# Kernel tuning notes

Hardware: AMD Instinct MI355X
Metric: run time of the kernel (lower is better)

The kernel has to match this reference:

```python
import jax, jax.numpy as jnp
import numpy as np
from jax import lax

N, G, L, D, E, STEPS = 65536, 128, 512, 128, 262144, 6
C = 2 * D  # concat dim (input_dim + output_dim)


def setup_inputs() -> dict:
    key = jax.random.key(0)
    ks = jax.random.split(key, 12)
    sD = 1.0 / float(np.sqrt(D))
    sC = 1.0 / float(np.sqrt(C))
    return {
        "x": jax.random.normal(ks[0], (N, D), jnp.float32),
        "edge_index": jax.random.randint(ks[1], (2, E), 0, N, dtype=jnp.int32),
        "edge_weight": jax.random.uniform(ks[2], (E,), jnp.float32),
        "batch": (jnp.arange(N) // L).astype(jnp.int32),  # sorted graph ids, L nodes/graph
        "ggnn_w": jax.random.normal(ks[3], (STEPS, D, D), jnp.float32) * sD,
        "gru_wih": jax.random.normal(ks[4], (3 * D, D), jnp.float32) * sD,
        "gru_whh": jax.random.normal(ks[5], (3 * D, D), jnp.float32) * sD,
        "gru_bih": jnp.zeros((3 * D,), jnp.float32),
        "gru_bhh": jnp.zeros((3 * D,), jnp.float32),
        "conv1_w": jax.random.normal(ks[6], (D, D, 3), jnp.float32) * sD,
        "conv1_b": jnp.zeros((D,), jnp.float32),
        "conv2_w": jax.random.normal(ks[7], (D, D, 1), jnp.float32) * sD,
        "conv2_b": jnp.zeros((D,), jnp.float32),
        "convc1_w": jax.random.normal(ks[8], (C, C, 3), jnp.float32) * sC,
        "convc1_b": jnp.zeros((C,), jnp.float32),
        "convc2_w": jax.random.normal(ks[9], (C, C, 1), jnp.float32) * sC,
        "convc2_b": jnp.zeros((C,), jnp.float32),
        "bn1_g": jnp.ones((D,), jnp.float32),
        "bn1_b": jnp.zeros((D,), jnp.float32),
        "bn2_g": jnp.ones((C,), jnp.float32),
        "bn2_b": jnp.zeros((C,), jnp.float32),
        "mlpy_w": jax.random.normal(ks[10], (2, D), jnp.float32) * sD,
        "mlpy_b": jnp.zeros((2,), jnp.float32),
        "mlpz_w": jax.random.normal(ks[11], (2, C), jnp.float32) * sC,
        "mlpz_b": jnp.zeros((2,), jnp.float32),
    }


def _gru(m, h, wih, whh, bih, bhh):
    gx = m @ wih.T + bih
    gh = h @ whh.T + bhh
    xr, xz, xn = jnp.split(gx, 3, axis=-1)
    hr, hz, hn = jnp.split(gh, 3, axis=-1)
    r = jax.nn.sigmoid(xr + hr)
    z = jax.nn.sigmoid(xz + hz)
    n = jnp.tanh(xn + r * hn)
    return (1.0 - z) * n + z * h


def _conv1d(x, w, b):  # x [G,Cin,L], w [Cout,Cin,K]
    y = lax.conv_general_dilated(x, w, (1,), "VALID", dimension_numbers=("NCH", "OIH", "NCH"))
    return y + b[None, :, None]


def _maxpool(x, k, s):
    return lax.reduce_window(x, -jnp.inf, lax.max, (1, 1, k), (1, 1, s), "VALID")


def _bn(x, g, b):  # training-mode BatchNorm1d over (N, L) per channel
    mean = x.mean(axis=(0, 2), keepdims=True)
    var = x.var(axis=(0, 2), keepdims=True)
    return (x - mean) * lax.rsqrt(var + 1e-5) * g[None, :, None] + b[None, :, None]


def reference(x, edge_index, edge_weight, batch, ggnn_w, gru_wih, gru_whh, gru_bih,
              gru_bhh, conv1_w, conv1_b, conv2_w, conv2_b, convc1_w, convc1_b,
              convc2_w, convc2_b, bn1_g, bn1_b, bn2_g, bn2_b, mlpy_w, mlpy_b,
              mlpz_w, mlpz_b):
    src, dst = edge_index[0], edge_index[1]

    # GatedGraphConv: per layer linear -> weighted message scatter-add -> GRU update
    def step(h, w):
        m = h @ w
        agg = jax.ops.segment_sum(m[src] * edge_weight[:, None], dst, num_segments=N)
        return _gru(agg, h, gru_wih, gru_whh, gru_bih, gru_bhh), None

    h, _ = lax.scan(step, x, ggnn_w)

    # de_batchify_graphs: one fused scatter into zero-padded [G, L, *] tensor
    counts = jax.ops.segment_sum(jnp.ones((N,), jnp.int32), batch, num_segments=G)
    offsets = jnp.cumsum(counts) - counts
    pos = jnp.arange(N) - offsets[batch]
    x_i = jnp.zeros((G, L, D), x.dtype).at[batch, pos].set(x)
    h_i = jnp.zeros((G, L, D), h.dtype).at[batch, pos].set(h)
    c_i = jnp.concatenate([h_i, x_i], axis=-1)  # [G, L, 2D]

    hT = h_i.transpose(0, 2, 1)  # [G, D, L]
    Y1 = _maxpool(jax.nn.relu(_bn(_conv1d(hT, conv1_w, conv1_b), bn1_g, bn1_b)), 3, 2)
    Y2 = _maxpool(jax.nn.relu(_bn(_conv1d(Y1, conv2_w, conv2_b), bn1_g, bn1_b)), 2, 2).transpose(0, 2, 1)
    cT = c_i.transpose(0, 2, 1)  # [G, 2D, L]
    Z1 = _maxpool(jax.nn.relu(_bn(_conv1d(cT, convc1_w, convc1_b), bn2_g, bn2_b)), 3, 2)
    Z2 = _maxpool(jax.nn.relu(_bn(_conv1d(Z1, convc2_w, convc2_b), bn2_g, bn2_b)), 2, 2).transpose(0, 2, 1)

    before_avg = (Y2 @ mlpy_w.T + mlpy_b) * (Z2 @ mlpz_w.T + mlpz_b)  # [G, L', 2]
    return before_avg.mean(axis=1)  # [G, 2]
```

## Files before the change

### kernel.cpp

```cpp
#include <hip/hip_runtime.h>
#include <math.h>

#define NN 65536
#define GG 128
#define LL 512
#define DD 128
#define EE 262144
#define NSTEPS 6
#define CC 256
#define L1 510
#define P1 254
#define P2 127

typedef __attribute__((ext_vector_type(8))) short s8bf;
typedef __attribute__((ext_vector_type(4))) float f4acc;

__device__ __forceinline__ unsigned short f2bf(float x) {
  unsigned u = __float_as_uint(x);
  unsigned r = u + 0x7FFFu + ((u >> 16) & 1u);
  return (unsigned short)(r >> 16);
}
__device__ __forceinline__ float bf2f(unsigned short h) {
  return __uint_as_float(((unsigned)h) << 16);
}
__device__ __forceinline__ unsigned short f2bf_sel(float x, int lo_sel) {
  unsigned short hi = f2bf(x);
  if (!lo_sel) return hi;
  return f2bf(x - bf2f(hi));
}
__device__ __forceinline__ uint2 pack4bf(float4 v, int lo_sel) {
  unsigned short s0 = f2bf_sel(v.x, lo_sel), s1 = f2bf_sel(v.y, lo_sel);
  unsigned short s2 = f2bf_sel(v.z, lo_sel), s3 = f2bf_sel(v.w, lo_sel);
  uint2 pk; pk.x = (unsigned)s0 | ((unsigned)s1 << 16);
  pk.y = (unsigned)s2 | ((unsigned)s3 << 16);
  return pk;
}

__global__ __launch_bounds__(256) void k_prep(
    const float* __restrict__ wih, const float* __restrict__ whh,
    const float* __restrict__ gw,
    const float* __restrict__ w1, const float* __restrict__ wc1,
    const float* __restrict__ w2, const float* __restrict__ wc2,
    unsigned short* __restrict__ wihCh, unsigned short* __restrict__ wihCl,
    unsigned short* __restrict__ whhCh, unsigned short* __restrict__ whhCl,
    unsigned short* __restrict__ gwTh, unsigned short* __restrict__ gwTl,
    unsigned short* __restrict__ c1h, unsigned short* __restrict__ c1l,
    unsigned short* __restrict__ cc1h, unsigned short* __restrict__ cc1l,
    unsigned short* __restrict__ c2h, unsigned short* __restrict__ c2l,
    unsigned short* __restrict__ cc2h, unsigned short* __restrict__ cc2l) {
  int i = blockIdx.x * 256 + threadIdx.x;
  if (i < 49152) {
    float v = wih[i];
    unsigned short h_ = f2bf(v);
    wihCh[i] = h_; wihCl[i] = f2bf(v - bf2f(h_));
    float u = whh[i];
    unsigned short h2 = f2bf(u);
    whhCh[i] = h2; whhCl[i] = f2bf(u - bf2f(h2));
  }
  if (i < 98304) {
    int s = i >> 14; int r = i & 16383; int c = r >> 7; int k = r & 127;
    float v = gw[(s << 14) + k * 128 + c];
    unsigned short h_ = f2bf(v);
    gwTh[i] = h_; gwTl[i] = f2bf(v - bf2f(h_));
  }
  if (i < 49152) {
    int ci = i & 127; int r = i >> 7; int co = r & 127; int tap = r >> 7;
    float v = w1[(co * 128 + ci) * 3 + tap];
    unsigned short h_ = f2bf(v);
    c1h[i] = h_; c1l[i] = f2bf(v - bf2f(h_));
  }
  if (i < 196608) {
    int ci = i & 255; int r = i >> 8; int co = r & 255; int tap = r >> 8;
    float v = wc1[(co * 256 + ci) * 3 + tap];
    unsigned short h_ = f2bf(v);
    cc1h[i] = h_; cc1l[i] = f2bf(v - bf2f(h_));
  }
  if (i < 16384) {
    float v = w2[i];
    unsigned short h_ = f2bf(v);
    c2h[i] = h_; c2l[i] = f2bf(v - bf2f(h_));
  }
  if (i < 65536) {
    float v = wc2[i];
    unsigned short h_ = f2bf(v);
    cc2h[i] = h_; cc2l[i] = f2bf(v - bf2f(h_));
  }
}

__global__ __launch_bounds__(256) void k_castx(const float* __restrict__ x,
                                               unsigned short* __restrict__ xH,
                                               unsigned short* __restrict__ xL) {
  int i = blockIdx.x * 256 + threadIdx.x;
  const float4* x4 = (const float4*)x;
  float4 a = x4[i * 2 + 0];
  float4 b = x4[i * 2 + 1];
  uint2 ha = pack4bf(a, 0), hb = pack4bf(b, 0);
  uint2 la = pack4bf(a, 1), lb = pack4bf(b, 1);
  uint4 hv; hv.x = ha.x; hv.y = ha.y; hv.z = hb.x; hv.w = hb.y;
  uint4 lv; lv.x = la.x; lv.y = la.y; lv.z = lb.x; lv.w = lb.y;
  *(uint4*)&xH[i * 8] = hv;
  *(uint4*)&xL[i * 8] = lv;
}

__global__ __launch_bounds__(256) void k_hist(const int* __restrict__ dst, int* __restrict__ cnt) {
  int e = blockIdx.x * 256 + threadIdx.x;
  if (e < EE) atomicAdd(&cnt[dst[e]], 1);
}

__global__ __launch_bounds__(1024) void k_scan(const int* __restrict__ cnt,
                                               int* __restrict__ rowptr,
                                               int* __restrict__ cursor) {
  __shared__ int part[1024];
  int t = threadIdx.x;
  int base = t * 64;
  int s = 0;
  for (int i = 0; i < 64; i++) s += cnt[base + i];
  part[t] = s;
  __syncthreads();
  for (int off = 1; off < 1024; off <<= 1) {
    int v = part[t];
    int u = (t >= off) ? part[t - off] : 0;
    __syncthreads();
    part[t] = v + u;
    __syncthreads();
  }
  int run = part[t] - s;
  for (int i = 0; i < 64; i++) {
    rowptr[base + i] = run;
    cursor[base + i] = run;
    run += cnt[base + i];
  }
  if (t == 1023) rowptr[NN] = run;
}

__global__ __launch_bounds__(256) void k_fill(const int* __restrict__ src,
                                              const int* __restrict__ dst,
                                              const float* __restrict__ ew,
                                              int* __restrict__ cursor,
                                              int* __restrict__ col,
                                              float* __restrict__ wgt) {
  int e = blockIdx.x * 256 + threadIdx.x;
  if (e < EE) {
    int d = dst[e];
    int p = atomicAdd(&cursor[d], 1);
    col[p] = src[e];
    wgt[p] = ew[e];
  }
}

__global__ __launch_bounds__(256, 4) void k_gemm_mfma(
    const unsigned short* __restrict__ Ah, const unsigned short* __restrict__ Al,
    const unsigned short* __restrict__ Wh, const unsigned short* __restrict__ Wl,
    float* __restrict__ Cout) {
  __shared__ __attribute__((aligned(16))) unsigned short As[64 * 136];
  int t = threadIdx.x;
  int r0 = blockIdx.x * 64;
  int wv = t >> 6, lane = t & 63;
  int ln = lane & 15, q = lane >> 4;
  f4acc acc[4][2];
#pragma unroll
  for (int mt = 0; mt < 4; mt++)
#pragma unroll
    for (int nt = 0; nt < 2; nt++) acc[mt][nt] = (f4acc)0.f;

  for (int p = 0; p < 3; p++) {
    if (p != 1) {
      const unsigned short* S = (p == 2) ? Al : Ah;
      if (p) __syncthreads();
#pragma unroll
      for (int it = 0; it < 4; it++) {
        int v8 = it * 256 + t;
        int row = v8 >> 4, k = (v8 & 15) * 8;
        *(uint4*)&As[row * 136 + k] = *(const uint4*)&S[(r0 + row) * 128 + k];
      }
      __syncthreads();
    }
    const unsigned short* W = (p == 1) ? Wl : Wh;
#pragma unroll
    for (int k0 = 0; k0 < 128; k0 += 32) {
      s8bf af[4], bf[2];
#pragma unroll
      for (int nt = 0; nt < 2; nt++)
        bf[nt] = *(const s8bf*)&W[(wv * 32 + nt * 16 + ln) * 128 + k0 + q * 8];
#pragma unroll
      for (int mt = 0; mt < 4; mt++)
        af[mt] = *(const s8bf*)&As[(mt * 16 + ln) * 136 + k0 + q * 8];
#pragma unroll
      for (int mt = 0; mt < 4; mt++)
#pragma unroll
        for (int nt = 0; nt < 2; nt++)
          acc[mt][nt] = __builtin_amdgcn_mfma_f32_16x16x32_bf16(af[mt], bf[nt], acc[mt][nt], 0, 0, 0);
    }
  }
#pragma unroll
  for (int mt = 0; mt < 4; mt++)
#pragma unroll
    for (int nt = 0; nt < 2; nt++)
#pragma unroll
      for (int reg = 0; reg < 4; reg++) {
        int r = r0 + mt * 16 + q * 4 + reg;
        Cout[r * 128 + wv * 32 + nt * 16 + ln] = acc[mt][nt][reg];
      }
}

__global__ __launch_bounds__(256) void k_gather(const float* __restrict__ m,
                                                const int* __restrict__ rowptr,
                                                const int* __restrict__ col,
                                                const float* __restrict__ wgt,
                                                unsigned short* __restrict__ aggH,
                                                unsigned short* __restrict__ aggL) {
  int t = threadIdx.x;
  int n = blockIdx.x * 8 + (t >> 5);
  int c4 = t & 31;
  const float4* m4 = (const float4*)m;
  int s0 = rowptr[n], s1 = rowptr[n + 1];
  float ax = 0.f, ay = 0.f, az = 0.f, aw = 0.f;
  int e = s0;
  for (; e + 2 <= s1; e += 2) {
    int cA = col[e], cB = col[e + 1];
    float wA = wgt[e], wB = wgt[e + 1];
    float4 vA = m4[cA * 32 + c4];
    float4 vB = m4[cB * 32 + c4];
    ax += vA.x * wA + vB.x * wB;
    ay += vA.y * wA + vB.y * wB;
    az += vA.z * wA + vB.z * wB;
    aw += vA.w * wA + vB.w * wB;
  }
  if (e < s1) {
    int cA = col[e];
    float wA = wgt[e];
    float4 vA = m4[cA * 32 + c4];
    ax += vA.x * wA; ay += vA.y * wA; az += vA.z * wA; aw += vA.w * wA;
  }
  unsigned short h0 = f2bf(ax), h1 = f2bf(ay), h2 = f2bf(az), h3 = f2bf(aw);
  unsigned short l0 = f2bf(ax - bf2f(h0)), l1 = f2bf(ay - bf2f(h1));
  unsigned short l2 = f2bf(az - bf2f(h2)), l3 = f2bf(aw - bf2f(h3));
  uint2 hpk, lpk;
  hpk.x = (unsigned)h0 | ((unsigned)h1 << 16); hpk.y = (unsigned)h2 | ((unsigned)h3 << 16);
  lpk.x = (unsigned)l0 | ((unsigned)l1 << 16); lpk.y = (unsigned)l2 | ((unsigned)l3 << 16);
  int base = n * 128 + c4 * 4;
  *(uint2*)&aggH[base] = hpk;
  *(uint2*)&aggL[base] = lpk;
}

__global__ __launch_bounds__(256, 2) void k_gru_mfma(
    const unsigned short* __restrict__ aggH, const unsigned short* __restrict__ aggL,
    const unsigned short* __restrict__ hinH, const unsigned short* __restrict__ hinL,
    const unsigned short* __restrict__ wihCh, const unsigned short* __restrict__ wihCl,
    const unsigned short* __restrict__ whhCh, const unsigned short* __restrict__ whhCl,
    const float* __restrict__ bih, const float* __restrict__ bhh,
    unsigned short* __restrict__ houtH, unsigned short* __restrict__ houtL) {
  __shared__ __attribute__((aligned(16))) unsigned short As[2 * 64 * 136];
  int t = threadIdx.x;
  int r0 = blockIdx.x * 64;
  int d0 = blockIdx.y * 64;
  int wv = t >> 6, lane = t & 63;
  int ln = lane & 15, q = lane >> 4;
  f4acc acc[4][6];
#pragma unroll
  for (int mt = 0; mt < 4; mt++)
#pragma unroll
    for (int tg = 0; tg < 6; tg++) acc[mt][tg] = (f4acc)0.f;

  for (int p = 0; p < 3; p++) {
    if (p != 1) {
      const unsigned short* s0 = (p == 2) ? aggL : aggH;
      const unsigned short* s1 = (p == 2) ? hinL : hinH;
      if (p) __syncthreads();
#pragma unroll
      for (int it = 0; it < 8; it++) {
        int v8 = it * 256 + t;
        int mat = v8 >> 10;
        int row = (v8 >> 4) & 63, k = (v8 & 15) * 8;
        const unsigned short* S = mat ? s1 : s0;
        *(uint4*)&As[mat * 8704 + row * 136 + k] = *(const uint4*)&S[(r0 + row) * 128 + k];
      }
      __syncthreads();
    }
    const unsigned short* wx = (p == 1) ? wihCl : wihCh;
    const unsigned short* wh = (p == 1) ? whhCl : whhCh;
#pragma unroll
    for (int k0 = 0; k0 < 128; k0 += 32) {
      s8bf af[2][4], bfr[6];
#pragma unroll
      for (int tg = 0; tg < 6; tg++) {
        int gate = (tg < 3) ? tg : tg - 3;
        const unsigned short* W = (tg < 3) ? wx : wh;
        bfr[tg] = *(const s8bf*)&W[(gate * 128 + d0 + wv * 16 + ln) * 128 + k0 + q * 8];
      }
#pragma unroll
      for (int mat = 0; mat < 2; mat++)
#pragma unroll
        for (int mt = 0; mt < 4; mt++)
          af[mat][mt] = *(const s8bf*)&As[mat * 8704 + (mt * 16 + ln) * 136 + k0 + q * 8];
#pragma unroll
      for (int mt = 0; mt < 4; mt++)
#pragma unroll
        for (int tg = 0; tg < 6; tg++)
          acc[mt][tg] = __builtin_amdgcn_mfma_f32_16x16x32_bf16(
              af[tg < 3 ? 0 : 1][mt], bfr[tg], acc[mt][tg], 0, 0, 0);
    }
  }
  int d = d0 + wv * 16 + ln;
  float bi0 = bih[d], bi1 = bih[128 + d], bi2 = bih[256 + d];
  float bh0 = bhh[d], bh1 = bhh[128 + d], bh2 = bhh[256 + d];
#pragma unroll
  for (int mt = 0; mt < 4; mt++) {
#pragma unroll
    for (int reg = 0; reg < 4; reg++) {
      int r = r0 + mt * 16 + q * 4 + reg;
      int idx = r * 128 + d;
      float hold = bf2f(hinH[idx]) + bf2f(hinL[idx]);
      float xr = acc[mt][0][reg] + bi0;
      float xz = acc[mt][1][reg] + bi1;
      float xn = acc[mt][2][reg] + bi2;
      float hr = acc[mt][3][reg] + bh0;
      float hz = acc[mt][4][reg] + bh1;
      float hn = acc[mt][5][reg] + bh2;
      float rr = 1.f / (1.f + expf(-(xr + hr)));
      float zz = 1.f / (1.f + expf(-(xz + hz)));
      float nnv = tanhf(xn + rr * hn);
      float hv = (1.f - zz) * nnv + zz * hold;
      unsigned short hh = f2bf(hv);
      houtH[idx] = hh;
      houtL[idx] = f2bf(hv - bf2f(hh));
    }
  }
}

template<int CIN, int TAPS, int WA>
__global__ __launch_bounds__(256, 4) void k_conv_mfma(
    const unsigned short* __restrict__ hiA, const unsigned short* __restrict__ hiB,
    const unsigned short* __restrict__ loA, const unsigned short* __restrict__ loB,
    const unsigned short* __restrict__ Wh, const unsigned short* __restrict__ Wl,
    const float* __restrict__ bias, float* __restrict__ out,
    float* __restrict__ stats, int Lin, int Lco) {
  constexpr int APAD = CIN + 8;
  constexpr int ROWS = 64 + TAPS - 1;
  constexpr int NCH = CIN / 32;
  constexpr int TOT8 = ROWS * CIN / 8;
  constexpr int NIT = (TOT8 + 255) / 256;
  constexpr int NINNER = TAPS * NCH;
  __shared__ __attribute__((aligned(16))) unsigned short As[ROWS * APAD];
  __shared__ float sred[256];
  const int g = blockIdx.z, co0 = blockIdx.y * 128, l0 = blockIdx.x * 64;
  const int t = threadIdx.x;
  const int wv = t >> 6, lane = t & 63, ln = lane & 15, q = lane >> 4;
  f4acc acc[4][2];
#pragma unroll
  for (int mt = 0; mt < 4; mt++)
#pragma unroll
    for (int nt = 0; nt < 2; nt++) acc[mt][nt] = (f4acc)0.f;

  for (int p = 0; p < 3; p++) {
    if (p != 1) {
      const unsigned short* pA = (p == 2) ? loA : hiA;
      const unsigned short* pB = (p == 2) ? loB : hiB;
      if (p) __syncthreads();
#pragma unroll
      for (int it = 0; it < NIT; it++) {
        int v8 = it * 256 + t;
        if (NIT * 256 == TOT8 || v8 < TOT8) {
          int row = (v8 * 8) / CIN, ch = (v8 * 8) % CIN;
          int lr = l0 + row; if (lr > Lin - 1) lr = Lin - 1;
          uint4 v;
          if (ch < WA) v = *(const uint4*)&pA[(g * Lin + lr) * WA + ch];
          else         v = *(const uint4*)&pB[(g * Lin + lr) * WA + ch - WA];
          *(uint4*)&As[row * APAD + ch] = v;
        }
      }
      __syncthreads();
    }
    const unsigned short* W = (p == 1) ? Wl : Wh;
    s8bf bcur[2], bnxt[2];
#pragma unroll
    for (int nt = 0; nt < 2; nt++)
      bcur[nt] = *(const s8bf*)&W[(co0 + wv * 32 + nt * 16 + ln) * CIN + q * 8];
#pragma unroll
    for (int it = 0; it < NINNER; it++) {
      const int tap = it / NCH, ch = it % NCH;
      if (it + 1 < NINNER) {
        const int ntap = (it + 1) / NCH, nch = (it + 1) % NCH;
#pragma unroll
        for (int nt = 0; nt < 2; nt++)
          bnxt[nt] = *(const s8bf*)&W[(ntap * CIN + co0 + wv * 32 + nt * 16 + ln) * CIN + nch * 32 + q * 8];
      }
      const int c0 = ch * 32;
      s8bf af[4];
#pragma unroll
      for (int mt = 0; mt < 4; mt++)
        af[mt] = *(const s8bf*)&As[(mt * 16 + ln + tap) * APAD + c0 + q * 8];
#pragma unroll
      for (int mt = 0; mt < 4; mt++)
#pragma unroll
        for (int nt = 0; nt < 2; nt++)
          acc[mt][nt] = __builtin_amdgcn_mfma_f32_16x16x32_bf16(af[mt], bcur[nt], acc[mt][nt], 0, 0, 0);
      if (it + 1 < NINNER) { bcur[0] = bnxt[0]; bcur[1] = bnxt[1]; }
    }
  }
  sred[t] = 0.f;
  __syncthreads();
#pragma unroll
  for (int nt = 0; nt < 2; nt++) {
    int cl = wv * 32 + nt * 16 + ln;
    int co = co0 + cl;
    float bv = bias[co];
    float s = 0.f, s2 = 0.f;
#pragma unroll
    for (int mt = 0; mt < 4; mt++)
#pragma unroll
      for (int reg = 0; reg < 4; reg++) {
        int l = l0 + mt * 16 + q * 4 + reg;
        if (l < Lco) {
          float v = acc[mt][nt][reg] + bv;
          out[(g * Lco + l) * CIN + co] = v;
          s += v; s2 += v * v;
        }
      }
    atomicAdd(&sred[cl], s);
    atomicAdd(&sred[128 + cl], s2);
  }
  __syncthreads();
  if (t < 128) atomicAdd(&stats[co0 + t], sred[t]);
  else atomicAdd(&stats[CIN + co0 + (t - 128)], sred[t]);
}

template<bool PLANES>
__global__ __launch_bounds__(256) void k_bnpool(const float* __restrict__ in,
                                                float* __restrict__ outF,
                                                unsigned short* __restrict__ outH,
                                                unsigned short* __restrict__ outL,
                                                const float* __restrict__ stats,
                                                const float* __restrict__ gamma,
                                                const float* __restrict__ beta,
                                                int Cch, int LinC, int Lout, int pk) {
  int idx = blockIdx.x * 256 + threadIdx.x;
  int total = GG * Cch * Lout;
  if (idx >= total) return;
  int c = idx & (Cch - 1);
  int r = idx / Cch;
  int p = r % Lout;
  int g = r / Lout;
  float cntf = (float)(GG * LinC);
  float mean = stats[c] / cntf;
  float var = stats[Cch + c] / cntf - mean * mean;
  float inv = rsqrtf(var + 1e-5f) * gamma[c];
  float sh = beta[c] - mean * inv;
  const float* base = &in[((g * LinC) + 2 * p) * Cch + c];
  float m = 0.f;
  for (int k = 0; k < pk; k++) {
    float v = fmaxf(base[k * Cch] * inv + sh, 0.f);
    m = fmaxf(m, v);
  }
  int o = (g * Lout + p) * Cch + c;
  if (PLANES) {
    unsigned short hh = f2bf(m);
    outH[o] = hh;
    outL[o] = f2bf(m - bf2f(hh));
  } else {
    outF[o] = m;
  }
}

__global__ __launch_bounds__(128) void k_final(const float* __restrict__ Y2,
                                               const float* __restrict__ Z2,
                                               const float* __restrict__ myw,
                                               const float* __restrict__ myb,
                                               const float* __restrict__ mzw,
                                               const float* __restrict__ mzb,
                                               float* __restrict__ outp) {
  __shared__ float red0[128];
  __shared__ float red1[128];
  int g = blockIdx.x;
  int t = threadIdx.x;
  float y0 = myb[0], y1 = myb[1], z0 = mzb[0], z1 = mzb[1];
  if (t < P2) {
    const float* yb = &Y2[(g * P2 + t) * 128];
    for (int c = 0; c < 128; c++) {
      float v = yb[c];
      y0 += v * myw[c];
      y1 += v * myw[128 + c];
    }
    const float* zb = &Z2[(g * P2 + t) * 256];
    for (int c = 0; c < 256; c++) {
      float v = zb[c];
      z0 += v * mzw[c];
      z1 += v * mzw[256 + c];
    }
  }
  red0[t] = (t < P2) ? y0 * z0 : 0.f;
  red1[t] = (t < P2) ? y1 * z1 : 0.f;
  __syncthreads();
  for (int off = 64; off > 0; off >>= 1) {
    if (t < off) {
      red0[t] += red0[t + off];
      red1[t] += red1[t + off];
    }
    __syncthreads();
  }
  if (t == 0) {
    outp[g * 2 + 0] = red0[0] / 127.f;
    outp[g * 2 + 1] = red1[0] / 127.f;
  }
}

extern "C" void kernel_launch(void* const* d_in, const int* in_sizes, int n_in,
                              void* d_out, int out_size, void* d_ws, size_t ws_size,
                              hipStream_t stream) {
  const float* x   = (const float*)d_in[0];
  const int* ei    = (const int*)d_in[1];
  const float* ew  = (const float*)d_in[2];
  const float* gw  = (const float*)d_in[4];
  const float* wih = (const float*)d_in[5];
  const float* whh = (const float*)d_in[6];
  const float* bih = (const float*)d_in[7];
  const float* bhh = (const float*)d_in[8];
  const float* w1  = (const float*)d_in[9];
  const float* b1  = (const float*)d_in[10];
  const float* w2  = (const float*)d_in[11];
  const float* b2  = (const float*)d_in[12];
  const float* wc1 = (const float*)d_in[13];
  const float* bc1 = (const float*)d_in[14];
  const float* wc2 = (const float*)d_in[15];
  const float* bc2 = (const float*)d_in[16];
  const float* bn1g = (const float*)d_in[17];
  const float* bn1b = (const float*)d_in[18];
  const float* bn2g = (const float*)d_in[19];
  const float* bn2b = (const float*)d_in[20];
  const float* myw = (const float*)d_in[21];
  const float* myb = (const float*)d_in[22];
  const float* mzw = (const float*)d_in[23];
  const float* mzb = (const float*)d_in[24];
  float* out = (float*)d_out;

  float* ws = (float*)d_ws;
  unsigned short* PH = (unsigned short*)ws;
  unsigned short* PL = PH + 8388608;
  unsigned short* xH = PL + 8388608;
  unsigned short* xL = xH + 8388608;
  unsigned short* c1h  = xL + 8388608;
  unsigned short* c1l  = c1h + 49152;
  unsigned short* cc1h = c1l + 49152;
  unsigned short* cc1l = cc1h + 196608;
  unsigned short* c2h  = cc1l + 196608;
  unsigned short* c2l  = c2h + 16384;
  unsigned short* cc2h = c2l + 16384;
  unsigned short* cc2l = cc2h + 65536;
  float* stats = (float*)(cc2l + 65536);
  float* Y2 = stats + 512;
  float* Z2 = Y2 + 2080768;
  float* shared0 = Z2 + 4161536;
  unsigned short* QH = (unsigned short*)shared0;
  unsigned short* QL = QH + 8388608;
  float* m = (float*)(QL + 8388608);
  unsigned short* aggH = (unsigned short*)(m + 8388608);
  unsigned short* aggL = aggH + 8388608;
  unsigned short* wihCh = aggL + 8388608;
  unsigned short* wihCl = wihCh + 49152;
  unsigned short* whhCh = wihCl + 49152;
  unsigned short* whhCl = whhCh + 49152;
  unsigned short* gwTh = whhCl + 49152;
  unsigned short* gwTl = gwTh + 98304;
  int* cnt    = (int*)(gwTl + 98304);
  int* rowptr = cnt + 65536;
  int* cursor = rowptr + 65537;
  int* col    = cursor + 65536;
  float* wgt  = (float*)(col + 262144);
  float* ggnn_end = wgt + 262144;
  float* bufA = shared0;
  unsigned short* bufBH = (unsigned short*)(bufA + 16711680);
  unsigned short* bufBL = bufBH + 8323072;
  float* conv_end = (float*)(bufBL + 8323072);
  float* wend = (ggnn_end > conv_end) ? ggnn_end : conv_end;
  size_t needed = (size_t)(wend - ws) * 4;
  if (ws_size < needed) return;

  const int* src = ei;
  const int* dst = ei + EE;

  k_prep<<<768, 256, 0, stream>>>(wih, whh, gw, w1, wc1, w2, wc2,
                                  wihCh, wihCl, whhCh, whhCl, gwTh, gwTl,
                                  c1h, c1l, cc1h, cc1l, c2h, c2l, cc2h, cc2l);
  k_castx<<<4096, 256, 0, stream>>>(x, xH, xL);
  hipMemsetAsync(cnt, 0, 65536 * 4, stream);
  k_hist<<<1024, 256, 0, stream>>>(dst, cnt);
  k_scan<<<1, 1024, 0, stream>>>(cnt, rowptr, cursor);
  k_fill<<<1024, 256, 0, stream>>>(src, dst, ew, cursor, col, wgt);

  for (int s = 0; s < NSTEPS; s++) {
    const unsigned short* AH = (s == 0) ? xH : ((s & 1) ? QH : PH);
    const unsigned short* AL = (s == 0) ? xL : ((s & 1) ? QL : PL);
    unsigned short* OH = (s & 1) ? PH : QH;
    unsigned short* OL = (s & 1) ? PL : QL;
    k_gemm_mfma<<<1024, 256, 0, stream>>>(AH, AL, gwTh + s * 16384, gwTl + s * 16384, m);
    k_gather<<<8192, 256, 0, stream>>>(m, rowptr, col, wgt, aggH, aggL);
    k_gru_mfma<<<dim3(1024, 2), 256, 0, stream>>>(aggH, aggL, AH, AL, wihCh, wihCl,
                                                  whhCh, whhCl, bih, bhh, OH, OL);
  }

  hipMemsetAsync(stats, 0, 512 * 4, stream);
  k_conv_mfma<128, 3, 128><<<dim3(8, 1, 128), 256, 0, stream>>>(
      PH, nullptr, PL, nullptr, c1h, c1l, b1, bufA, stats, 512, L1);
  k_bnpool<true><<<(GG * 128 * P1 + 255) / 256, 256, 0, stream>>>(
      bufA, nullptr, bufBH, bufBL, stats, bn1g, bn1b, 128, L1, P1, 3);
  hipMemsetAsync(stats, 0, 512 * 4, stream);
  k_conv_mfma<128, 1, 128><<<dim3(4, 1, 128), 256, 0, stream>>>(
      bufBH, nullptr, bufBL, nullptr, c2h, c2l, b2, bufA, stats, P1, P1);
  k_bnpool<false><<<(GG * 128 * P2 + 255) / 256, 256, 0, stream>>>(
      bufA, Y2, nullptr, nullptr, stats, bn1g, bn1b, 128, P1, P2, 2);

  hipMemsetAsync(stats, 0, 512 * 4, stream);
  k_conv_mfma<256, 3, 128><<<dim3(8, 2, 128), 256, 0, stream>>>(
      PH, xH, PL, xL, cc1h, cc1l, bc1, bufA, stats, 512, L1);
  k_bnpool<true><<<(GG * 256 * P1 + 255) / 256, 256, 0, stream>>>(
      bufA, nullptr, bufBH, bufBL, stats, bn2g, bn2b, 256, L1, P1, 3);
  hipMemsetAsync(stats, 0, 512 * 4, stream);
  k_conv_mfma<256, 1, 256><<<dim3(4, 2, 128), 256, 0, stream>>>(
      bufBH, nullptr, bufBL, nullptr, cc2h, cc2l, bc2, bufA, stats, P1, P1);
  k_bnpool<false><<<(GG * 256 * P2 + 255) / 256, 256, 0, stream>>>(
      bufA, Z2, nullptr, nullptr, stats, bn2g, bn2b, 256, P1, P2, 2);

  k_final<<<128, 128, 0, stream>>>(Y2, Z2, myw, myb, mzw, mzb, out);
}
```

Baseline: 1.580 ms.

## Swizzle LDS tiles and retile MFMA warps in GEMM, GRU and conv kernels

Replaces padded shared-memory tiles with XOR-swizzled unpadded layouts in the GEMM, GRU and conv kernels, avoiding LDS bank conflicts without padding. Warps are rearranged into a 2x2 (or 1x4) grid so each wave covers more output columns with fewer row tiles. This changes the balance between A-fragment and B-fragment loads. The 256-channel convolutions now compute all output channels in one block instead of splitting across blockIdx.y, which removes the redundant staging of the input tile. In exchange they carry more accumulators per thread, launch half as many blocks, and lower the occupancy hint to 3.

```diff
diff --git a/kernel.cpp b/kernel.cpp
--- a/kernel.cpp
+++ b/kernel.cpp
@@ -152,16 +152,17 @@
     const unsigned short* __restrict__ Ah, const unsigned short* __restrict__ Al,
     const unsigned short* __restrict__ Wh, const unsigned short* __restrict__ Wl,
     float* __restrict__ Cout) {
-  __shared__ __attribute__((aligned(16))) unsigned short As[64 * 136];
+  __shared__ __attribute__((aligned(16))) unsigned short As[64 * 128];
   int t = threadIdx.x;
   int r0 = blockIdx.x * 64;
   int wv = t >> 6, lane = t & 63;
   int ln = lane & 15, q = lane >> 4;
-  f4acc acc[4][2];
-#pragma unroll
-  for (int mt = 0; mt < 4; mt++)
-#pragma unroll
-    for (int nt = 0; nt < 2; nt++) acc[mt][nt] = (f4acc)0.f;
+  int wr = wv & 1, wc = wv >> 1;
+  f4acc acc[2][4];
+#pragma unroll
+  for (int mt = 0; mt < 2; mt++)
+#pragma unroll
+    for (int nt = 0; nt < 4; nt++) acc[mt][nt] = (f4acc)0.f;
 
   for (int p = 0; p < 3; p++) {
     if (p != 1) {
@@ -170,36 +171,40 @@
 #pragma unroll
       for (int it = 0; it < 4; it++) {
         int v8 = it * 256 + t;
-        int row = v8 >> 4, k = (v8 & 15) * 8;
-        *(uint4*)&As[row * 136 + k] = *(const uint4*)&S[(r0 + row) * 128 + k];
+        int row = v8 >> 4, gch = v8 & 15;
+        *(uint4*)&As[row * 128 + ((gch ^ (row & 7)) << 3)] =
+            *(const uint4*)&S[(r0 + row) * 128 + (gch << 3)];
       }
       __syncthreads();
     }
     const unsigned short* W = (p == 1) ? Wl : Wh;
 #pragma unroll
     for (int k0 = 0; k0 < 128; k0 += 32) {
-      s8bf af[4], bf[2];
-#pragma unroll
-      for (int nt = 0; nt < 2; nt++)
-        bf[nt] = *(const s8bf*)&W[(wv * 32 + nt * 16 + ln) * 128 + k0 + q * 8];
-#pragma unroll
-      for (int mt = 0; mt < 4; mt++)
-        af[mt] = *(const s8bf*)&As[(mt * 16 + ln) * 136 + k0 + q * 8];
-#pragma unroll
-      for (int mt = 0; mt < 4; mt++)
-#pragma unroll
-        for (int nt = 0; nt < 2; nt++)
+      s8bf af[2], bf[4];
+#pragma unroll
+      for (int nt = 0; nt < 4; nt++)
+        bf[nt] = *(const s8bf*)&W[(wc * 64 + nt * 16 + ln) * 128 + k0 + q * 8];
+#pragma unroll
+      for (int mt = 0; mt < 2; mt++) {
+        int row = wr * 32 + mt * 16 + ln;
+        int ck = ((k0 >> 3) + q) ^ (ln & 7);
+        af[mt] = *(const s8bf*)&As[row * 128 + (ck << 3)];
+      }
+#pragma unroll
+      for (int mt = 0; mt < 2; mt++)
+#pragma unroll
+        for (int nt = 0; nt < 4; nt++)
           acc[mt][nt] = __builtin_amdgcn_mfma_f32_16x16x32_bf16(af[mt], bf[nt], acc[mt][nt], 0, 0, 0);
     }
   }
 #pragma unroll
-  for (int mt = 0; mt < 4; mt++)
-#pragma unroll
-    for (int nt = 0; nt < 2; nt++)
+  for (int mt = 0; mt < 2; mt++)
+#pragma unroll
+    for (int nt = 0; nt < 4; nt++)
 #pragma unroll
       for (int reg = 0; reg < 4; reg++) {
-        int r = r0 + mt * 16 + q * 4 + reg;
-        Cout[r * 128 + wv * 32 + nt * 16 + ln] = acc[mt][nt][reg];
+        int r = r0 + wr * 32 + mt * 16 + q * 4 + reg;
+        Cout[r * 128 + wc * 64 + nt * 16 + ln] = acc[mt][nt][reg];
       }
 }
 
@@ -250,30 +255,34 @@
     const unsigned short* __restrict__ whhCh, const unsigned short* __restrict__ whhCl,
     const float* __restrict__ bih, const float* __restrict__ bhh,
     unsigned short* __restrict__ houtH, unsigned short* __restrict__ houtL) {
-  __shared__ __attribute__((aligned(16))) unsigned short As[2 * 64 * 136];
+  __shared__ __attribute__((aligned(16))) unsigned short As[2 * 64 * 128];
   int t = threadIdx.x;
   int r0 = blockIdx.x * 64;
   int d0 = blockIdx.y * 64;
   int wv = t >> 6, lane = t & 63;
   int ln = lane & 15, q = lane >> 4;
-  f4acc acc[4][6];
-#pragma unroll
-  for (int mt = 0; mt < 4; mt++)
-#pragma unroll
-    for (int tg = 0; tg < 6; tg++) acc[mt][tg] = (f4acc)0.f;
+  int wr = wv & 1, wc = wv >> 1;
+  f4acc acc[2][6][2];
+#pragma unroll
+  for (int mt = 0; mt < 2; mt++)
+#pragma unroll
+    for (int tg = 0; tg < 6; tg++)
+#pragma unroll
+      for (int nt = 0; nt < 2; nt++) acc[mt][tg][nt] = (f4acc)0.f;
 
   for (int p = 0; p < 3; p++) {
     if (p != 1) {
-      const unsigned short* s0 = (p == 2) ? aggL : aggH;
-      const unsigned short* s1 = (p == 2) ? hinL : hinH;
+      const unsigned short* sA = (p == 2) ? aggL : aggH;
+      const unsigned short* sB = (p == 2) ? hinL : hinH;
       if (p) __syncthreads();
 #pragma unroll
       for (int it = 0; it < 8; it++) {
         int v8 = it * 256 + t;
         int mat = v8 >> 10;
-        int row = (v8 >> 4) & 63, k = (v8 & 15) * 8;
-        const unsigned short* S = mat ? s1 : s0;
-        *(uint4*)&As[mat * 8704 + row * 136 + k] = *(const uint4*)&S[(r0 + row) * 128 + k];
+        int row = (v8 >> 4) & 63, gch = v8 & 15;
+        const unsigned short* S = mat ? sB : sA;
+        *(uint4*)&As[mat * 8192 + row * 128 + ((gch ^ (row & 7)) << 3)] =
+            *(const uint4*)&S[(r0 + row) * 128 + (gch << 3)];
       }
       __syncthreads();
     }
@@ -281,76 +290,89 @@
     const unsigned short* wh = (p == 1) ? whhCl : whhCh;
 #pragma unroll
     for (int k0 = 0; k0 < 128; k0 += 32) {
-      s8bf af[2][4], bfr[6];
+      s8bf af[2][2], bfr[6][2];
 #pragma unroll
       for (int tg = 0; tg < 6; tg++) {
         int gate = (tg < 3) ? tg : tg - 3;
         const unsigned short* W = (tg < 3) ? wx : wh;
-        bfr[tg] = *(const s8bf*)&W[(gate * 128 + d0 + wv * 16 + ln) * 128 + k0 + q * 8];
+#pragma unroll
+        for (int nt = 0; nt < 2; nt++)
+          bfr[tg][nt] = *(const s8bf*)&W[(gate * 128 + d0 + wc * 32 + nt * 16 + ln) * 128 + k0 + q * 8];
       }
 #pragma unroll
       for (int mat = 0; mat < 2; mat++)
 #pragma unroll
-        for (int mt = 0; mt < 4; mt++)
-          af[mat][mt] = *(const s8bf*)&As[mat * 8704 + (mt * 16 + ln) * 136 + k0 + q * 8];
-#pragma unroll
-      for (int mt = 0; mt < 4; mt++)
+        for (int mt = 0; mt < 2; mt++) {
+          int row = wr * 32 + mt * 16 + ln;
+          int ck = ((k0 >> 3) + q) ^ (ln & 7);
+          af[mat][mt] = *(const s8bf*)&As[mat * 8192 + row * 128 + (ck << 3)];
+        }
+#pragma unroll
+      for (int mt = 0; mt < 2; mt++)
 #pragma unroll
         for (int tg = 0; tg < 6; tg++)
-          acc[mt][tg] = __builtin_amdgcn_mfma_f32_16x16x32_bf16(
-              af[tg < 3 ? 0 : 1][mt], bfr[tg], acc[mt][tg], 0, 0, 0);
-    }
-  }
-  int d = d0 + wv * 16 + ln;
-  float bi0 = bih[d], bi1 = bih[128 + d], bi2 = bih[256 + d];
-  float bh0 = bhh[d], bh1 = bhh[128 + d], bh2 = bhh[256 + d];
-#pragma unroll
-  for (int mt = 0; mt < 4; mt++) {
-#pragma unroll
-    for (int reg = 0; reg < 4; reg++) {
-      int r = r0 + mt * 16 + q * 4 + reg;
-      int idx = r * 128 + d;
-      float hold = bf2f(hinH[idx]) + bf2f(hinL[idx]);
-      float xr = acc[mt][0][reg] + bi0;
-      float xz = acc[mt][1][reg] + bi1;
-      float xn = acc[mt][2][reg] + bi2;
-      float hr = acc[mt][3][reg] + bh0;
-      float hz = acc[mt][4][reg] + bh1;
-      float hn = acc[mt][5][reg] + bh2;
-      float rr = 1.f / (1.f + expf(-(xr + hr)));
-      float zz = 1.f / (1.f + expf(-(xz + hz)));
-      float nnv = tanhf(xn + rr * hn);
-      float hv = (1.f - zz) * nnv + zz * hold;
-      unsigned short hh = f2bf(hv);
-      houtH[idx] = hh;
-      houtL[idx] = f2bf(hv - bf2f(hh));
+#pragma unroll
+          for (int nt = 0; nt < 2; nt++)
+            acc[mt][tg][nt] = __builtin_amdgcn_mfma_f32_16x16x32_bf16(
+                af[tg < 3 ? 0 : 1][mt], bfr[tg][nt], acc[mt][tg][nt], 0, 0, 0);
+    }
+  }
+#pragma unroll
+  for (int nt = 0; nt < 2; nt++) {
+    int d = d0 + wc * 32 + nt * 16 + ln;
+    float bi0 = bih[d], bi1 = bih[128 + d], bi2 = bih[256 + d];
+    float bh0 = bhh[d], bh1 = bhh[128 + d], bh2 = bhh[256 + d];
+#pragma unroll
+    for (int mt = 0; mt < 2; mt++) {
+#pragma unroll
+      for (int reg = 0; reg < 4; reg++) {
+        int r = r0 + wr * 32 + mt * 16 + q * 4 + reg;
+        int idx = r * 128 + d;
+        float hold = bf2f(hinH[idx]) + bf2f(hinL[idx]);
+        float xr = acc[mt][0][nt][reg] + bi0;
+        float xz = acc[mt][1][nt][reg] + bi1;
+        float xn = acc[mt][2][nt][reg] + bi2;
+        float hr = acc[mt][3][nt][reg] + bh0;
+        float hz = acc[mt][4][nt][reg] + bh1;
+        float hn = acc[mt][5][nt][reg] + bh2;
+        float rr = 1.f / (1.f + expf(-(xr + hr)));
+        float zz = 1.f / (1.f + expf(-(xz + hz)));
+        float nnv = tanhf(xn + rr * hn);
+        float hv = (1.f - zz) * nnv + zz * hold;
+        unsigned short hh = f2bf(hv);
+        houtH[idx] = hh;
+        houtL[idx] = f2bf(hv - bf2f(hh));
+      }
     }
   }
 }
 
 template<int CIN, int TAPS, int WA>
-__global__ __launch_bounds__(256, 4) void k_conv_mfma(
+__global__ __launch_bounds__(256, (CIN == 128) ? 4 : 3) void k_conv_mfma(
     const unsigned short* __restrict__ hiA, const unsigned short* __restrict__ hiB,
     const unsigned short* __restrict__ loA, const unsigned short* __restrict__ loB,
     const unsigned short* __restrict__ Wh, const unsigned short* __restrict__ Wl,
     const float* __restrict__ bias, float* __restrict__ out,
     float* __restrict__ stats, int Lin, int Lco) {
-  constexpr int APAD = CIN + 8;
   constexpr int ROWS = 64 + TAPS - 1;
   constexpr int NCH = CIN / 32;
-  constexpr int TOT8 = ROWS * CIN / 8;
+  constexpr int CHUNKS = CIN / 8;
+  constexpr int TOT8 = ROWS * CHUNKS;
   constexpr int NIT = (TOT8 + 255) / 256;
   constexpr int NINNER = TAPS * NCH;
-  __shared__ __attribute__((aligned(16))) unsigned short As[ROWS * APAD];
-  __shared__ float sred[256];
-  const int g = blockIdx.z, co0 = blockIdx.y * 128, l0 = blockIdx.x * 64;
+  constexpr int MT = (CIN == 128) ? 2 : 4;
+  __shared__ __attribute__((aligned(16))) unsigned short As[ROWS * CIN];
+  __shared__ float sred[2 * CIN];
+  const int g = blockIdx.z, l0 = blockIdx.x * 64;
   const int t = threadIdx.x;
   const int wv = t >> 6, lane = t & 63, ln = lane & 15, q = lane >> 4;
-  f4acc acc[4][2];
-#pragma unroll
-  for (int mt = 0; mt < 4; mt++)
-#pragma unroll
-    for (int nt = 0; nt < 2; nt++) acc[mt][nt] = (f4acc)0.f;
+  const int wr = (CIN == 128) ? (wv & 1) : 0;
+  const int wc = (CIN == 128) ? (wv >> 1) : wv;
+  f4acc acc[MT][4];
+#pragma unroll
+  for (int mt = 0; mt < MT; mt++)
+#pragma unroll
+    for (int nt = 0; nt < 4; nt++) acc[mt][nt] = (f4acc)0.f;
 
   for (int p = 0; p < 3; p++) {
     if (p != 1) {
@@ -361,68 +383,72 @@
       for (int it = 0; it < NIT; it++) {
         int v8 = it * 256 + t;
         if (NIT * 256 == TOT8 || v8 < TOT8) {
-          int row = (v8 * 8) / CIN, ch = (v8 * 8) % CIN;
+          int row = v8 / CHUNKS, gch = v8 % CHUNKS;
+          int ch = gch * 8;
           int lr = l0 + row; if (lr > Lin - 1) lr = Lin - 1;
           uint4 v;
           if (ch < WA) v = *(const uint4*)&pA[(g * Lin + lr) * WA + ch];
           else         v = *(const uint4*)&pB[(g * Lin + lr) * WA + ch - WA];
-          *(uint4*)&As[row * APAD + ch] = v;
+          *(uint4*)&As[row * CIN + ((gch ^ (row & 7)) << 3)] = v;
         }
       }
       __syncthreads();
     }
     const unsigned short* W = (p == 1) ? Wl : Wh;
-    s8bf bcur[2], bnxt[2];
-#pragma unroll
-    for (int nt = 0; nt < 2; nt++)
-      bcur[nt] = *(const s8bf*)&W[(co0 + wv * 32 + nt * 16 + ln) * CIN + q * 8];
+    s8bf bcur[4], bnxt[4];
+#pragma unroll
+    for (int nt = 0; nt < 4; nt++)
+      bcur[nt] = *(const s8bf*)&W[(wc * 64 + nt * 16 + ln) * CIN + q * 8];
 #pragma unroll
     for (int it = 0; it < NINNER; it++) {
-      const int tap = it / NCH, ch = it % NCH;
+      const int tap = it / NCH, chh = it % NCH;
       if (it + 1 < NINNER) {
         const int ntap = (it + 1) / NCH, nch = (it + 1) % NCH;
 #pragma unroll
-        for (int nt = 0; nt < 2; nt++)
-          bnxt[nt] = *(const s8bf*)&W[(ntap * CIN + co0 + wv * 32 + nt * 16 + ln) * CIN + nch * 32 + q * 8];
-      }
-      const int c0 = ch * 32;
-      s8bf af[4];
-#pragma unroll
-      for (int mt = 0; mt < 4; mt++)
-        af[mt] = *(const s8bf*)&As[(mt * 16 + ln + tap) * APAD + c0 + q * 8];
-#pragma unroll
-      for (int mt = 0; mt < 4; mt++)
-#pragma unroll
-        for (int nt = 0; nt < 2; nt++)
+        for (int nt = 0; nt < 4; nt++)
+          bnxt[nt] = *(const s8bf*)&W[(ntap * CIN + wc * 64 + nt * 16 + ln) * CIN + nch * 32 + q * 8];
+      }
+      s8bf af[MT];
+#pragma unroll
+      for (int mt = 0; mt < MT; mt++) {
+        int row = wr * 32 + mt * 16 + ln + tap;
+        int ck = (chh * 4 + q) ^ ((ln + tap) & 7);
+        af[mt] = *(const s8bf*)&As[row * CIN + (ck << 3)];
+      }
+#pragma unroll
+      for (int mt = 0; mt < MT; mt++)
+#pragma unroll
+        for (int nt = 0; nt < 4; nt++)
           acc[mt][nt] = __builtin_amdgcn_mfma_f32_16x16x32_bf16(af[mt], bcur[nt], acc[mt][nt], 0, 0, 0);
-      if (it + 1 < NINNER) { bcur[0] = bnxt[0]; bcur[1] = bnxt[1]; }
-    }
-  }
-  sred[t] = 0.f;
+      if (it + 1 < NINNER) {
+#pragma unroll
+        for (int nt = 0; nt < 4; nt++) bcur[nt] = bnxt[nt];
+      }
+    }
+  }
+  for (int i = t; i < 2 * CIN; i += 256) sred[i] = 0.f;
   __syncthreads();
 #pragma unroll
-  for (int nt = 0; nt < 2; nt++) {
-    int cl = wv * 32 + nt * 16 + ln;
-    int co = co0 + cl;
-    float bv = bias[co];
+  for (int nt = 0; nt < 4; nt++) {
+    int cl = wc * 64 + nt * 16 + ln;
+    float bv = bias[cl];
     float s = 0.f, s2 = 0.f;
 #pragma unroll
-    for (int mt = 0; mt < 4; mt++)
+    for (int mt = 0; mt < MT; mt++)
 #pragma unroll
       for (int reg = 0; reg < 4; reg++) {
-        int l = l0 + mt * 16 + q * 4 + reg;
+        int l = l0 + wr * 32 + mt * 16 + q * 4 + reg;
         if (l < Lco) {
           float v = acc[mt][nt][reg] + bv;
-          out[(g * Lco + l) * CIN + co] = v;
+          out[(g * Lco + l) * CIN + cl] = v;
           s += v; s2 += v * v;
         }
       }
     atomicAdd(&sred[cl], s);
-    atomicAdd(&sred[128 + cl], s2);
+    atomicAdd(&sred[CIN + cl], s2);
   }
   __syncthreads();
-  if (t < 128) atomicAdd(&stats[co0 + t], sred[t]);
-  else atomicAdd(&stats[CIN + co0 + (t - 128)], sred[t]);
+  for (int i = t; i < 2 * CIN; i += 256) atomicAdd(&stats[i], sred[i]);
 }
 
 template<bool PLANES>
@@ -610,12 +636,12 @@
       bufA, Y2, nullptr, nullptr, stats, bn1g, bn1b, 128, P1, P2, 2);
 
   hipMemsetAsync(stats, 0, 512 * 4, stream);
-  k_conv_mfma<256, 3, 128><<<dim3(8, 2, 128), 256, 0, stream>>>(
+  k_conv_mfma<256, 3, 128><<<dim3(8, 1, 128), 256, 0, stream>>>(
       PH, xH, PL, xL, cc1h, cc1l, bc1, bufA, stats, 512, L1);
   k_bnpool<true><<<(GG * 256 * P1 + 255) / 256, 256, 0, stream>>>(
       bufA, nullptr, bufBH, bufBL, stats, bn2g, bn2b, 256, L1, P1, 3);
   hipMemsetAsync(stats, 0, 512 * 4, stream);
-  k_conv_mfma<256, 1, 256><<<dim3(4, 2, 128), 256, 0, stream>>>(
+  k_conv_mfma<256, 1, 256><<<dim3(4, 1, 128), 256, 0, stream>>>(
       bufBH, nullptr, bufBL, nullptr, cc2h, cc2l, bc2, bufA, stats, P1, P1);
   k_bnpool<false><<<(GG * 256 * P2 + 255) / 256, 256, 0, stream>>>(
       bufA, Z2, nullptr, nullptr, stats, bn2g, bn2b, 256, P1, P2, 2);
```

New measurement: 2.016 ms. 1.28x slower.

## Split conv K dimension into halves to shrink LDS tile; unroll gather by four

Applied to the files above, without the earlier changes.

The conv MFMA kernel now stages only half of the input channels in shared memory at a time and loops over four segments (hi/lo activation × two K halves) instead of three passes over the full width. This halves the LDS footprint per block so more blocks can be resident at the intended 4 per CU, especially for the CIN=256 variant. The cost is more barriers and more reloads of the tile per block. Separately, the edge gather loop is unrolled to four edges per iteration so more independent row loads are in flight.

```diff
diff --git a/kernel.cpp b/kernel.cpp
--- a/kernel.cpp
+++ b/kernel.cpp
@@ -216,17 +216,19 @@
   int s0 = rowptr[n], s1 = rowptr[n + 1];
   float ax = 0.f, ay = 0.f, az = 0.f, aw = 0.f;
   int e = s0;
-  for (; e + 2 <= s1; e += 2) {
-    int cA = col[e], cB = col[e + 1];
-    float wA = wgt[e], wB = wgt[e + 1];
+  for (; e + 4 <= s1; e += 4) {
+    int cA = col[e], cB = col[e + 1], cC = col[e + 2], cD = col[e + 3];
+    float wA = wgt[e], wB = wgt[e + 1], wC = wgt[e + 2], wD = wgt[e + 3];
     float4 vA = m4[cA * 32 + c4];
     float4 vB = m4[cB * 32 + c4];
-    ax += vA.x * wA + vB.x * wB;
-    ay += vA.y * wA + vB.y * wB;
-    az += vA.z * wA + vB.z * wB;
-    aw += vA.w * wA + vB.w * wB;
-  }
-  if (e < s1) {
+    float4 vC = m4[cC * 32 + c4];
+    float4 vD = m4[cD * 32 + c4];
+    ax += vA.x * wA + vB.x * wB + vC.x * wC + vD.x * wD;
+    ay += vA.y * wA + vB.y * wB + vC.y * wC + vD.y * wD;
+    az += vA.z * wA + vB.z * wB + vC.z * wC + vD.z * wD;
+    aw += vA.w * wA + vB.w * wB + vC.w * wC + vD.w * wD;
+  }
+  for (; e < s1; e++) {
     int cA = col[e];
     float wA = wgt[e];
     float4 vA = m4[cA * 32 + c4];
@@ -335,12 +337,14 @@
     const unsigned short* __restrict__ Wh, const unsigned short* __restrict__ Wl,
     const float* __restrict__ bias, float* __restrict__ out,
     float* __restrict__ stats, int Lin, int Lco) {
-  constexpr int APAD = CIN + 8;
+  constexpr int KH = CIN / 2;
+  constexpr int APAD = KH + 8;
   constexpr int ROWS = 64 + TAPS - 1;
-  constexpr int NCH = CIN / 32;
-  constexpr int TOT8 = ROWS * CIN / 8;
+  constexpr int NCHH = KH / 32;
+  constexpr int CHUNKS = KH / 8;
+  constexpr int TOT8 = ROWS * CHUNKS;
   constexpr int NIT = (TOT8 + 255) / 256;
-  constexpr int NINNER = TAPS * NCH;
+  constexpr int NINNER = TAPS * NCHH;
   __shared__ __attribute__((aligned(16))) unsigned short As[ROWS * APAD];
   __shared__ float sred[256];
   const int g = blockIdx.z, co0 = blockIdx.y * 128, l0 = blockIdx.x * 64;
@@ -352,50 +356,53 @@
 #pragma unroll
     for (int nt = 0; nt < 2; nt++) acc[mt][nt] = (f4acc)0.f;
 
-  for (int p = 0; p < 3; p++) {
-    if (p != 1) {
-      const unsigned short* pA = (p == 2) ? loA : hiA;
-      const unsigned short* pB = (p == 2) ? loB : hiB;
-      if (p) __syncthreads();
-#pragma unroll
-      for (int it = 0; it < NIT; it++) {
-        int v8 = it * 256 + t;
-        if (NIT * 256 == TOT8 || v8 < TOT8) {
-          int row = (v8 * 8) / CIN, ch = (v8 * 8) % CIN;
-          int lr = l0 + row; if (lr > Lin - 1) lr = Lin - 1;
-          uint4 v;
-          if (ch < WA) v = *(const uint4*)&pA[(g * Lin + lr) * WA + ch];
-          else         v = *(const uint4*)&pB[(g * Lin + lr) * WA + ch - WA];
-          *(uint4*)&As[row * APAD + ch] = v;
+  for (int seg = 0; seg < 4; seg++) {
+    const int alo = seg >> 1;
+    const int kh = seg & 1;
+    const unsigned short* pA = alo ? loA : hiA;
+    const unsigned short* pB = alo ? loB : hiB;
+    if (seg) __syncthreads();
+#pragma unroll
+    for (int it = 0; it < NIT; it++) {
+      int v8 = it * 256 + t;
+      if (NIT * 256 == TOT8 || v8 < TOT8) {
+        int row = v8 / CHUNKS, chl = (v8 % CHUNKS) * 8;
+        int ch = kh * KH + chl;
+        int lr = l0 + row; if (lr > Lin - 1) lr = Lin - 1;
+        uint4 v;
+        if (ch < WA) v = *(const uint4*)&pA[(g * Lin + lr) * WA + ch];
+        else         v = *(const uint4*)&pB[(g * Lin + lr) * WA + ch - WA];
+        *(uint4*)&As[row * APAD + chl] = v;
+      }
+    }
+    __syncthreads();
+    const int nb = alo ? 1 : 2;
+    for (int b = 0; b < nb; b++) {
+      const unsigned short* W = b ? Wl : Wh;
+      s8bf bcur[2], bnxt[2];
+#pragma unroll
+      for (int nt = 0; nt < 2; nt++)
+        bcur[nt] = *(const s8bf*)&W[(co0 + wv * 32 + nt * 16 + ln) * CIN + kh * KH + q * 8];
+#pragma unroll
+      for (int it = 0; it < NINNER; it++) {
+        const int tap = it / NCHH, cc = it % NCHH;
+        if (it + 1 < NINNER) {
+          const int ntap = (it + 1) / NCHH, ncc = (it + 1) % NCHH;
+#pragma unroll
+          for (int nt = 0; nt < 2; nt++)
+            bnxt[nt] = *(const s8bf*)&W[(ntap * CIN + co0 + wv * 32 + nt * 16 + ln) * CIN + kh * KH + ncc * 32 + q * 8];
         }
+        s8bf af[4];
+#pragma unroll
+        for (int mt = 0; mt < 4; mt++)
+          af[mt] = *(const s8bf*)&As[(mt * 16 + ln + tap) * APAD + cc * 32 + q * 8];
+#pragma unroll
+        for (int mt = 0; mt < 4; mt++)
+#pragma unroll
+          for (int nt = 0; nt < 2; nt++)
+            acc[mt][nt] = __builtin_amdgcn_mfma_f32_16x16x32_bf16(af[mt], bcur[nt], acc[mt][nt], 0, 0, 0);
+        if (it + 1 < NINNER) { bcur[0] = bnxt[0]; bcur[1] = bnxt[1]; }
       }
-      __syncthreads();
-    }
-    const unsigned short* W = (p == 1) ? Wl : Wh;
-    s8bf bcur[2], bnxt[2];
-#pragma unroll
-    for (int nt = 0; nt < 2; nt++)
-      bcur[nt] = *(const s8bf*)&W[(co0 + wv * 32 + nt * 16 + ln) * CIN + q * 8];
-#pragma unroll
-    for (int it = 0; it < NINNER; it++) {
-      const int tap = it / NCH, ch = it % NCH;
-      if (it + 1 < NINNER) {
-        const int ntap = (it + 1) / NCH, nch = (it + 1) % NCH;
-#pragma unroll
-        for (int nt = 0; nt < 2; nt++)
-          bnxt[nt] = *(const s8bf*)&W[(ntap * CIN + co0 + wv * 32 + nt * 16 + ln) * CIN + nch * 32 + q * 8];
-      }
-      const int c0 = ch * 32;
-      s8bf af[4];
-#pragma unroll
-      for (int mt = 0; mt < 4; mt++)
-        af[mt] = *(const s8bf*)&As[(mt * 16 + ln + tap) * APAD + c0 + q * 8];
-#pragma unroll
-      for (int mt = 0; mt < 4; mt++)
-#pragma unroll
-        for (int nt = 0; nt < 2; nt++)
-          acc[mt][nt] = __builtin_amdgcn_mfma_f32_16x16x32_bf16(af[mt], bcur[nt], acc[mt][nt], 0, 0, 0);
-      if (it + 1 < NINNER) { bcur[0] = bnxt[0]; bcur[1] = bnxt[1]; }
     }
   }
   sred[t] = 0.f;
```

Result: slower. 1.987 ms (+25.8%).
